# Kernel optimization log

Hardware: AMD Instinct MI355X
Metric: run time of the kernel (lower is better)

The kernel has to match this reference:

```python
import jax, jax.numpy as jnp
import numpy as np

B, N, D, H = 4, 1024, 768, 12
HD = D // H
HID = 4 * D
EPS = 1e-5


def setup_inputs():
    key = jax.random.key(0)
    ks = iter(jax.random.split(key, 64))
    def rnd(*shape):
        return jax.random.normal(next(ks), shape, jnp.float32) * 0.02
    d = {
        "img_tok": jax.random.normal(next(ks), (B, N, D), jnp.float32),
        "evt_tok": jax.random.normal(next(ks), (B, N, D), jnp.float32),
    }
    for nm in ["ln_q1", "ln_kv1", "ln_q2", "ln_kv2", "ln_mi", "ln_me"]:
        d[nm + "_g"] = jnp.ones((D,), jnp.float32)
        d[nm + "_b"] = jnp.zeros((D,), jnp.float32)
    for p in ["si", "se"]:
        d[p + "_qkv_w"] = rnd(D, 3 * D)
        d[p + "_qkv_b"] = jnp.zeros((3 * D,), jnp.float32)
        d[p + "_proj_w"] = rnd(D, D)
        d[p + "_proj_b"] = jnp.zeros((D,), jnp.float32)
    for p in ["xei", "xie"]:
        for m in ["q", "k", "v", "p"]:
            d[p + "_" + m + "_w"] = rnd(D, D)
            d[p + "_" + m + "_b"] = jnp.zeros((D,), jnp.float32)
    for p in ["mi", "me"]:
        d[p + "_fc1_w"] = rnd(D, HID)
        d[p + "_fc1_b"] = jnp.zeros((HID,), jnp.float32)
        d[p + "_fc2_w"] = rnd(HID, D)
        d[p + "_fc2_b"] = jnp.zeros((D,), jnp.float32)
    return d


def _ln(x, g, b):
    m = jnp.mean(x, -1, keepdims=True)
    v = jnp.mean((x - m) ** 2, -1, keepdims=True)
    return (x - m) * jax.lax.rsqrt(v + EPS) * g + b


def _self_attn(x, qkv_w, qkv_b, p_w, p_b):
    qkv = (x @ qkv_w + qkv_b).reshape(B, N, 3, H, HD)
    q, k, v = qkv[:, :, 0], qkv[:, :, 1], qkv[:, :, 2]  # each (B,N,H,HD)
    s = jnp.einsum("bqhd,bkhd->bhqk", q, k) * (HD ** -0.5)
    a = jax.nn.softmax(s, -1)
    o = jnp.einsum("bhqk,bkhd->bqhd", a, v).reshape(B, N, D)
    return o @ p_w + p_b


def _cross_attn(qx, kvx, q_w, q_b, k_w, k_b, v_w, v_b, p_w, p_b):
    q = (qx @ q_w + q_b).reshape(B, N, H, HD)
    k = (kvx @ k_w + k_b).reshape(B, N, H, HD)
    v = (kvx @ v_w + v_b).reshape(B, N, H, HD)
    # invert_softmax=True: negate scores before softmax
    s = -(jnp.einsum("bqhd,bkhd->bhqk", q, k) * (HD ** -0.5))
    a = jax.nn.softmax(s, -1)
    o = jnp.einsum("bhqk,bkhd->bqhd", a, v).reshape(B, N, D)
    return o @ p_w + p_b


def _mlp(x, w1, b1, w2, b2):
    return jax.nn.gelu(x @ w1 + b1, approximate=False) @ w2 + b2


def _fwd(img_tok, evt_tok,
         ln_q1_g, ln_q1_b, ln_kv1_g, ln_kv1_b,
         si_qkv_w, si_qkv_b, si_proj_w, si_proj_b,
         se_qkv_w, se_qkv_b, se_proj_w, se_proj_b,
         ln_q2_g, ln_q2_b, ln_kv2_g, ln_kv2_b,
         xei_q_w, xei_q_b, xei_k_w, xei_k_b, xei_v_w, xei_v_b, xei_p_w, xei_p_b,
         xie_q_w, xie_q_b, xie_k_w, xie_k_b, xie_v_w, xie_v_b, xie_p_w, xie_p_b,
         ln_mi_g, ln_mi_b, mi_fc1_w, mi_fc1_b, mi_fc2_w, mi_fc2_b,
         ln_me_g, ln_me_b, me_fc1_w, me_fc1_b, me_fc2_w, me_fc2_b):
    img = img_tok + _self_attn(_ln(img_tok, ln_q1_g, ln_q1_b),
                               si_qkv_w, si_qkv_b, si_proj_w, si_proj_b)
    evt = evt_tok + _self_attn(_ln(evt_tok, ln_kv1_g, ln_kv1_b),
                               se_qkv_w, se_qkv_b, se_proj_w, se_proj_b)
    i1, e1 = img, evt
    # shared norm_q2 / norm_kv2 weights across both cross-attn directions
    img = i1 + _cross_attn(_ln(i1, ln_q2_g, ln_q2_b), _ln(e1, ln_kv2_g, ln_kv2_b),
                           xei_q_w, xei_q_b, xei_k_w, xei_k_b, xei_v_w, xei_v_b,
                           xei_p_w, xei_p_b)
    evt = e1 + _cross_attn(_ln(e1, ln_q2_g, ln_q2_b), _ln(i1, ln_kv2_g, ln_kv2_b),
                           xie_q_w, xie_q_b, xie_k_w, xie_k_b, xie_v_w, xie_v_b,
                           xie_p_w, xie_p_b)
    img = img + _mlp(_ln(img, ln_mi_g, ln_mi_b), mi_fc1_w, mi_fc1_b, mi_fc2_w, mi_fc2_b)
    evt = evt + _mlp(_ln(evt, ln_me_g, ln_me_b), me_fc1_w, me_fc1_b, me_fc2_w, me_fc2_b)
    return img, evt


def reference(img_tok, evt_tok,
              ln_q1_g, ln_q1_b, ln_kv1_g, ln_kv1_b,
              si_qkv_w, si_qkv_b, si_proj_w, si_proj_b,
              se_qkv_w, se_qkv_b, se_proj_w, se_proj_b,
              ln_q2_g, ln_q2_b, ln_kv2_g, ln_kv2_b,
              xei_q_w, xei_q_b, xei_k_w, xei_k_b, xei_v_w, xei_v_b, xei_p_w, xei_p_b,
              xie_q_w, xie_q_b, xie_k_w, xie_k_b, xie_v_w, xie_v_b, xie_p_w, xie_p_b,
              ln_mi_g, ln_mi_b, mi_fc1_w, mi_fc1_b, mi_fc2_w, mi_fc2_b,
              ln_me_g, ln_me_b, me_fc1_w, me_fc1_b, me_fc2_w, me_fc2_b):
    return _fwd(img_tok, evt_tok,
                ln_q1_g, ln_q1_b, ln_kv1_g, ln_kv1_b,
                si_qkv_w, si_qkv_b, si_proj_w, si_proj_b,
                se_qkv_w, se_qkv_b, se_proj_w, se_proj_b,
                ln_q2_g, ln_q2_b, ln_kv2_g, ln_kv2_b,
                xei_q_w, xei_q_b, xei_k_w, xei_k_b, xei_v_w, xei_v_b, xei_p_w, xei_p_b,
                xie_q_w, xie_q_b, xie_k_w, xie_k_b, xie_v_w, xie_v_b, xie_p_w, xie_p_b,
                ln_mi_g, ln_mi_b, mi_fc1_w, mi_fc1_b, mi_fc2_w, mi_fc2_b,
                ln_me_g, ln_me_b, me_fc1_w, me_fc1_b, me_fc2_w, me_fc2_b)
```

## Files before the change

kernel.cpp:

```cpp
#include <hip/hip_runtime.h>

constexpr int cB  = 4;
constexpr int cN  = 1024;
constexpr int cD  = 768;
constexpr int cH  = 12;
constexpr int cHD = 64;
constexpr int cHID = 3072;
constexpr int cBN = cB * cN;

typedef __attribute__((ext_vector_type(8))) short bf16x8;
typedef __attribute__((ext_vector_type(4))) float f32x4;

static __device__ __forceinline__ unsigned short f2bf(float f) {
    union { float f; unsigned int u; } v; v.f = f;
    unsigned int u = v.u;
    return (unsigned short)((u + 0x7FFFu + ((u >> 16) & 1u)) >> 16);
}

static __device__ __forceinline__ float gelu_as(float v) {
    float w  = v * 0.70710678118f;
    float aw = fabsf(w);
    float t  = __builtin_amdgcn_rcpf(fmaf(aw, 0.3275911f, 1.0f));
    float p  = t * fmaf(t, fmaf(t, fmaf(t, fmaf(t, 1.061405429f, -1.453152027f),
                                        1.421413741f), -0.284496736f), 0.254829592f);
    float e  = __builtin_amdgcn_exp2f(w * w * -1.44269504f);
    float ea = fmaf(-p, e, 1.0f);
    float er = __builtin_copysignf(ea, w);
    return 0.5f * v * (1.0f + er);
}

static __device__ __forceinline__ void gl_lds16(const void* g, void* l) {
    __builtin_amdgcn_global_load_lds(
        (const __attribute__((address_space(1))) unsigned int*)g,
        (__attribute__((address_space(3))) unsigned int*)l, 16, 0, 0);
}

struct WcTab {
    const float* src[16];
    unsigned long long dstoff[16];
    int K[16];
    int N[16];
    int start[17];
};

__global__ __launch_bounds__(256)
void wconv_all(WcTab tab, unsigned short* __restrict__ WoBase) {
    int b = blockIdx.x;
    int i = 0;
    while (i < 15 && b >= tab.start[i + 1]) i++;
    const float* __restrict__ W = tab.src[i];
    unsigned short* __restrict__ Wo = WoBase + tab.dstoff[i];
    int K = tab.K[i], N = tab.N[i];
    int tb = b - tab.start[i];
    int Kt = K >> 6;
    int k0 = (tb % Kt) * 64, n0 = (tb / Kt) * 64;

    __shared__ float Ls[64][68];
    int t = threadIdx.x;
    int lr = t >> 4, lc = (t & 15) * 4;
    #pragma unroll
    for (int q = 0; q < 4; q++) {
        float4 v = *(const float4*)&W[(size_t)(k0 + lr + q * 16) * N + n0 + lc];
        Ls[lr + q * 16][lc + 0] = v.x;  Ls[lr + q * 16][lc + 1] = v.y;
        Ls[lr + q * 16][lc + 2] = v.z;  Ls[lr + q * 16][lc + 3] = v.w;
    }
    __syncthreads();
    int mt = t >> 3;
    int nb = mt & 3, kb = mt >> 2;
    int sub = t & 7;
    int K8 = K >> 3;
    size_t chunk = ((size_t)(n0 / 16 + nb) * K8 + (size_t)(k0 / 8 + kb)) * 128;
    unsigned short buf[16];
    #pragma unroll
    for (int rr = 0; rr < 2; rr++) {
        int n_r = sub * 2 + rr;
        #pragma unroll
        for (int kk = 0; kk < 8; kk++)
            buf[rr * 8 + kk] = f2bf(Ls[kb * 8 + kk][nb * 16 + n_r]);
    }
    uint4 w0, w1;
    w0.x = buf[0] | ((unsigned)buf[1] << 16);   w0.y = buf[2] | ((unsigned)buf[3] << 16);
    w0.z = buf[4] | ((unsigned)buf[5] << 16);   w0.w = buf[6] | ((unsigned)buf[7] << 16);
    w1.x = buf[8] | ((unsigned)buf[9] << 16);   w1.y = buf[10] | ((unsigned)buf[11] << 16);
    w1.z = buf[12] | ((unsigned)buf[13] << 16); w1.w = buf[14] | ((unsigned)buf[15] << 16);
    *(uint4*)&Wo[chunk + sub * 16]     = w0;
    *(uint4*)&Wo[chunk + sub * 16 + 8] = w1;
}

static __device__ __forceinline__ void ln_body(const float* __restrict__ x,
                                               const float* __restrict__ g,
                                               const float* __restrict__ b,
                                               unsigned short* __restrict__ y,
                                               int R) {
    __shared__ float psum[16][17], psq[16][17];
    __shared__ float mean_s[16], rstd_s[16];
    int t = threadIdx.x;
    int r = t >> 4, c16 = t & 15;
    const float* xr = x + ((size_t)R * 16 + r) * cD;
    float s = 0.f, sq = 0.f;
    #pragma unroll
    for (int i = 0; i < 12; i++) {
        float4 v = *(const float4*)&xr[c16 * 4 + i * 64];
        s  += v.x + v.y + v.z + v.w;
        sq += v.x * v.x + v.y * v.y + v.z * v.z + v.w * v.w;
    }
    psum[r][c16] = s; psq[r][c16] = sq;
    __syncthreads();
    if (t < 16) {
        float ss = 0.f, qq = 0.f;
        #pragma unroll
        for (int i = 0; i < 16; i++) { ss += psum[t][i]; qq += psq[t][i]; }
        float m = ss / (float)cD;
        mean_s[t] = m;
        rstd_s[t] = rsqrtf(qq / (float)cD - m * m + 1e-5f);
    }
    __syncthreads();
    int r2 = t & 15, cslot = t >> 4;
    const float* xr2 = x + ((size_t)R * 16 + r2) * cD;
    float m = mean_s[r2], rs = rstd_s[r2];
    for (int c = cslot; c < 96; c += 16) {
        float4 a0 = *(const float4*)&xr2[c * 8];
        float4 a1 = *(const float4*)&xr2[c * 8 + 4];
        float4 g0 = *(const float4*)&g[c * 8];
        float4 g1 = *(const float4*)&g[c * 8 + 4];
        float4 b0 = *(const float4*)&b[c * 8];
        float4 b1 = *(const float4*)&b[c * 8 + 4];
        unsigned short o[8];
        o[0] = f2bf((a0.x - m) * rs * g0.x + b0.x);
        o[1] = f2bf((a0.y - m) * rs * g0.y + b0.y);
        o[2] = f2bf((a0.z - m) * rs * g0.z + b0.z);
        o[3] = f2bf((a0.w - m) * rs * g0.w + b0.w);
        o[4] = f2bf((a1.x - m) * rs * g1.x + b1.x);
        o[5] = f2bf((a1.y - m) * rs * g1.y + b1.y);
        o[6] = f2bf((a1.z - m) * rs * g1.z + b1.z);
        o[7] = f2bf((a1.w - m) * rs * g1.w + b1.w);
        uint4 w;
        w.x = o[0] | ((unsigned)o[1] << 16); w.y = o[2] | ((unsigned)o[3] << 16);
        w.z = o[4] | ((unsigned)o[5] << 16); w.w = o[6] | ((unsigned)o[7] << 16);
        *(uint4*)&y[((size_t)R * 96 + c) * 128 + r2 * 8] = w;
    }
}

struct LnTab {
    const float* x[4];
    const float* g[4];
    const float* b[4];
    unsigned short* y[4];
};

__global__ __launch_bounds__(256)
void ln4_kernel(LnTab T) {
    int s = blockIdx.x >> 8;
    ln_body(T.x[s], T.g[s], T.b[s], T.y[s], blockIdx.x & 255);
}

struct GPair {
    const unsigned short* A0;  const unsigned short* A1;
    const unsigned short* B0;  const unsigned short* B1;
    const float* bias0;        const float* bias1;
    const float* biasB0;       const float* biasB1;
    const float* res0;         const float* res1;
    void* C0;                  void* C1;
    unsigned short* V0;        unsigned short* V1;
};

template<int NBUF, int KS>
__global__ __launch_bounds__(256, 4)
void mfma_gemm(GPair P, int K, int N, int ostride, int vsplit, int mode) {
    constexpr int KC   = KS / 8;
    constexpr int ASL  = 128 * KS / 8;
    constexpr int BSL  = 64 * KS / 8;
    constexpr int LPA  = ASL / 256;
    constexpr int LPB  = BSL / 256;
    constexpr int AH   = NBUF - 1;
    constexpr int NSUB = KS / 32;
    __shared__ bf16x8 aT[NBUF][ASL];
    __shared__ bf16x8 bT[NBUF][BSL];

    int z = blockIdx.z;
    const unsigned short* A   = z ? P.A1 : P.A0;
    const unsigned short* Bw  = z ? P.B1 : P.B0;
    const float* bias  = z ? P.bias1  : P.bias0;
    const float* biasB = z ? P.biasB1 : P.biasB0;
    const float* res   = z ? P.res1   : P.res0;
    void* Cout         = z ? P.C1     : P.C0;
    unsigned short* VtOut = z ? P.V1  : P.V0;

    int t = threadIdx.x;
    int w = t >> 6, l = t & 63;
    int la = l & 15, lb = l >> 4;
    int m0 = blockIdx.x * 128, n0 = blockIdx.y * 64;
    int K8 = K >> 3;

    f32x4 acc[2][4];
    #pragma unroll
    for (int i = 0; i < 2; i++)
        #pragma unroll
        for (int j = 0; j < 4; j++) acc[i][j] = (f32x4){0.f, 0.f, 0.f, 0.f};

    const unsigned short* pA[LPA];
    #pragma unroll
    for (int q = 0; q < LPA; q++) {
        int slot = w * (LPA * 64) + q * 64 + l;
        int ci = slot >> 4, sub = slot & 15;
        int mi = ci / KC, kb = ci % KC;
        pA[q] = A + (((size_t)((m0 >> 4) + mi)) * K8 + kb) * 128 + sub * 8;
    }
    const unsigned short* pB[LPB];
    #pragma unroll
    for (int q = 0; q < LPB; q++) {
        int slot = w * (LPB * 64) + q * 64 + l;
        int ci = slot >> 4, sub = slot & 15;
        int nj = ci / KC, kb = ci % KC;
        pB[q] = Bw + (((size_t)((n0 >> 4) + nj)) * K8 + kb) * 128 + sub * 8;
    }

    auto stage = [&](int buf, int step) {
        size_t off = (size_t)step * (KS * 16);
        #pragma unroll
        for (int q = 0; q < LPA; q++)
            gl_lds16(pA[q] + off, &aT[buf][w * (LPA * 64) + q * 64]);
        #pragma unroll
        for (int q = 0; q < LPB; q++)
            gl_lds16(pB[q] + off, &bT[buf][w * (LPB * 64) + q * 64]);
    };

    int nsteps = K / KS;
    #pragma unroll
    for (int p = 0; p < AH; p++) stage(p, p);
    for (int s = 0; s < nsteps; s++) {
        int cb = s % NBUF;
        int rem = nsteps - 1 - s;
        if (s + AH < nsteps) {
            stage((s + AH) % NBUF, s + AH);
            asm volatile("s_waitcnt vmcnt(6)" ::: "memory");
        } else if (rem == 2) {
            asm volatile("s_waitcnt vmcnt(6)" ::: "memory");
        } else if (rem == 1) {
            asm volatile("s_waitcnt vmcnt(3)" ::: "memory");
        } else {
            asm volatile("s_waitcnt vmcnt(0)" ::: "memory");
        }
        __builtin_amdgcn_s_barrier();

        #pragma unroll
        for (int kk = 0; kk < NSUB; kk++) {
            bf16x8 av[2], bv[4];
            #pragma unroll
            for (int i = 0; i < 2; i++)
                av[i] = aT[cb][((2 * w + i) * KC + kk * 4 + lb) * 16 + la];
            #pragma unroll
            for (int j = 0; j < 4; j++)
                bv[j] = bT[cb][(j * KC + kk * 4 + lb) * 16 + la];
            #pragma unroll
            for (int i = 0; i < 2; i++)
                #pragma unroll
                for (int j = 0; j < 4; j++)
                    acc[i][j] = __builtin_amdgcn_mfma_f32_16x16x32_bf16(av[i], bv[j], acc[i][j], 0, 0, 0);
        }

        asm volatile("s_waitcnt lgkmcnt(0)" ::: "memory");
        __builtin_amdgcn_s_barrier();
    }

    int col = l & 15;
    int rb = (l >> 4) * 4;
    int mw = m0 + w * 32;
    if (mode == 2) {
        float* out = (float*)Cout;
        #pragma unroll
        for (int j = 0; j < 4; j++) {
            int n = n0 + j * 16 + col;
            float bj = bias[n];
            #pragma unroll
            for (int i = 0; i < 2; i++)
                #pragma unroll
                for (int r = 0; r < 4; r++) {
                    int mm = mw + i * 16 + rb + r;
                    out[(size_t)mm * ostride + n] = acc[i][j][r] + bj + res[(size_t)mm * ostride + n];
                }
        }
    } else if (mode == 1) {
        unsigned short* out = (unsigned short*)Cout;
        int N8 = N >> 3;
        #pragma unroll
        for (int j = 0; j < 4; j++) {
            int n = n0 + j * 16 + col;
            float bj = bias[n];
            #pragma unroll
            for (int i = 0; i < 2; i++)
                #pragma unroll
                for (int r = 0; r < 4; r++) {
                    int mm = mw + i * 16 + rb + r;
                    float v = gelu_as(acc[i][j][r] + bj);
                    size_t ad = ((size_t)(mm >> 4) * N8 + (n >> 3)) * 128 + (mm & 15) * 8 + (n & 7);
                    out[ad] = f2bf(v);
                }
        }
    } else {
        bool toVt = (mode == 3) && (n0 >= vsplit);
        if (!toVt) {
            unsigned short* out = (unsigned short*)Cout;
            #pragma unroll
            for (int j = 0; j < 4; j++) {
                int n = n0 + j * 16 + col;
                float bj = bias[n];
                #pragma unroll
                for (int i = 0; i < 2; i++)
                    #pragma unroll
                    for (int r = 0; r < 4; r++) {
                        int mm = mw + i * 16 + rb + r;
                        out[(size_t)mm * ostride + n] = f2bf(acc[i][j][r] + bj);
                    }
            }
        } else {
            #pragma unroll
            for (int j = 0; j < 4; j++) {
                int n = n0 + j * 16 + col;
                int vc = n - vsplit;
                float bj = biasB[vc];
                int ph = vc >> 6, d = vc & 63;
                #pragma unroll
                for (int i = 0; i < 2; i++) {
                    int mm = mw + i * 16 + rb;
                    int bbv = mm >> 10, tok = mm & 1023;
                    unsigned short q0 = f2bf(acc[i][j][0] + bj);
                    unsigned short q1 = f2bf(acc[i][j][1] + bj);
                    unsigned short q2 = f2bf(acc[i][j][2] + bj);
                    unsigned short q3 = f2bf(acc[i][j][3] + bj);
                    uint2 pk;
                    pk.x = q0 | ((unsigned)q1 << 16);
                    pk.y = q2 | ((unsigned)q3 << 16);
                    size_t ad = ((size_t)(bbv * 12 + ph) * 64 + d) * 1024 + tok;
                    *(uint2*)&VtOut[ad] = pk;
                }
            }
        }
    }
}

__global__ __launch_bounds__(256, 2)
void fattn_kernel(const unsigned short* __restrict__ Q0,
                  const unsigned short* __restrict__ Q1,
                  const unsigned short* __restrict__ Kq0,
                  const unsigned short* __restrict__ Kq1,
                  const unsigned short* __restrict__ Vt0,
                  const unsigned short* __restrict__ Vt1,
                  unsigned short* __restrict__ Oo0,
                  unsigned short* __restrict__ Oo1,
                  int qk_stride, float scale) {
    __shared__ unsigned short Kls[2][4096];
    __shared__ unsigned short Vls[2][4096];
    __shared__ unsigned short Ps[4][16][72];

    int z = blockIdx.z;
    const unsigned short* Qp = z ? Q1 : Q0;
    const unsigned short* Kp = z ? Kq1 : Kq0;
    const unsigned short* Vt = z ? Vt1 : Vt0;
    unsigned short* O        = z ? Oo1 : Oo0;

    int t = threadIdx.x;
    int w = t >> 6, l = t & 63;
    int la = l & 15, lb = l >> 4;
    int swz = la & 7;
    int blk = blockIdx.x;
    int qt0 = (blk & 15) * 64 + w * 16;
    int bh = blk >> 4;
    int h = bh % cH, bb = bh / cH;

    const unsigned short* Qb = Qp + (size_t)(bb * cN) * qk_stride + h * cHD;
    const unsigned short* Kb = Kp + (size_t)(bb * cN) * qk_stride + h * cHD;
    const unsigned short* Vb = Vt + (size_t)(bb * cH + h) * (64 * 1024);

    bf16x8 av[2];
    #pragma unroll
    for (int s = 0; s < 2; s++)
        av[s] = *(const bf16x8*)(Qb + (size_t)(qt0 + la) * qk_stride + 32 * s + 8 * lb);

    int ch0 = w * 128 + l;
    int ch1 = ch0 + 64;
    int r0 = ch0 >> 3, c0 = (ch0 & 7) ^ (r0 & 7);
    int r1 = ch1 >> 3, c1 = (ch1 & 7) ^ (r1 & 7);
    const unsigned short* K0 = Kb + (size_t)r0 * qk_stride + c0 * 8;
    const unsigned short* K1 = Kb + (size_t)r1 * qk_stride + c1 * 8;
    const unsigned short* V0 = Vb + (size_t)r0 * 1024 + c0 * 8;
    const unsigned short* V1 = Vb + (size_t)r1 * 1024 + c1 * 8;
    int dst0 = w * 1024;
    int dst1 = dst0 + 512;

    auto stage = [&](int buf, int kt0) {
        gl_lds16(K0 + (size_t)kt0 * qk_stride, &Kls[buf][dst0]);
        gl_lds16(K1 + (size_t)kt0 * qk_stride, &Kls[buf][dst1]);
        gl_lds16(V0 + kt0, &Vls[buf][dst0]);
        gl_lds16(V1 + kt0, &Vls[buf][dst1]);
    };

    const float sc2 = scale * 1.44269504f;
    bf16x8 ones;
    #pragma unroll
    for (int e = 0; e < 8; e++) ones[e] = (short)0x3F80;

    float m2[4];
    f32x4 acc_o[4], acc_l;
    #pragma unroll
    for (int r = 0; r < 4; r++) m2[r] = -1e30f;
    acc_l = (f32x4){0.f, 0.f, 0.f, 0.f};
    #pragma unroll
    for (int nt = 0; nt < 4; nt++) acc_o[nt] = (f32x4){0.f, 0.f, 0.f, 0.f};

    stage(0, 0);
    for (int it = 0; it < 16; it++) {
        int cb = it & 1;
        if (it < 15) {
            stage(cb ^ 1, (it + 1) << 6);
            asm volatile("s_waitcnt vmcnt(4)" ::: "memory");
        } else {
            asm volatile("s_waitcnt vmcnt(0)" ::: "memory");
        }
        __builtin_amdgcn_s_barrier();
        asm volatile("" ::: "memory");

        bf16x8 kf[4][2];
        #pragma unroll
        for (int j = 0; j < 4; j++)
            #pragma unroll
            for (int s = 0; s < 2; s++)
                kf[j][s] = *(const bf16x8*)&Kls[cb][(16 * j + la) * 64 + (((4 * s + lb) ^ swz) << 3)];

        f32x4 sj[4];
        #pragma unroll
        for (int j = 0; j < 4; j++) sj[j] = (f32x4){0.f, 0.f, 0.f, 0.f};
        #pragma unroll
        for (int j = 0; j < 4; j++)
            #pragma unroll
            for (int s = 0; s < 2; s++)
                sj[j] = __builtin_amdgcn_mfma_f32_16x16x32_bf16(av[s], kf[j][s], sj[j], 0, 0, 0);

        float x2[4][4];
        #pragma unroll
        for (int j = 0; j < 4; j++)
            #pragma unroll
            for (int r = 0; r < 4; r++) x2[j][r] = sj[j][r] * sc2;

        float p[4][4];
        #pragma unroll
        for (int j = 0; j < 4; j++)
            #pragma unroll
            for (int r = 0; r < 4; r++)
                p[j][r] = __builtin_amdgcn_exp2f(x2[j][r] - m2[r]);

        float mt2[4];
        #pragma unroll
        for (int r = 0; r < 4; r++)
            mt2[r] = fmaxf(fmaxf(x2[0][r], x2[1][r]), fmaxf(x2[2][r], x2[3][r]));
        #pragma unroll
        for (int off = 1; off <= 8; off <<= 1)
            #pragma unroll
            for (int r = 0; r < 4; r++)
                mt2[r] = fmaxf(mt2[r], __shfl_xor(mt2[r], off, 64));

        int ok = (mt2[0] <= m2[0] + 11.f) && (mt2[1] <= m2[1] + 11.f) &&
                 (mt2[2] <= m2[2] + 11.f) && (mt2[3] <= m2[3] + 11.f);
        if (!__all(ok)) {
            #pragma unroll
            for (int r = 0; r < 4; r++) {
                float mn = fmaxf(m2[r], mt2[r]);
                float al = __builtin_amdgcn_exp2f(m2[r] - mn);
                acc_l[r] *= al;
                #pragma unroll
                for (int nt = 0; nt < 4; nt++) acc_o[nt][r] *= al;
                m2[r] = mn;
            }
            #pragma unroll
            for (int j = 0; j < 4; j++)
                #pragma unroll
                for (int r = 0; r < 4; r++)
                    p[j][r] = __builtin_amdgcn_exp2f(x2[j][r] - m2[r]);
        }

        #pragma unroll
        for (int j = 0; j < 4; j++)
            #pragma unroll
            for (int rp = 0; rp < 2; rp++) {
                unsigned u;
                asm("v_cvt_pk_bf16_f32 %0, %1, %2"
                    : "=v"(u) : "v"(p[j][2 * rp]), "v"(p[j][2 * rp + 1]));
                Ps[w][lb * 4 + 2 * rp][16 * j + la]     = (unsigned short)u;
                Ps[w][lb * 4 + 2 * rp + 1][16 * j + la] = (unsigned short)(u >> 16);
            }
        asm volatile("s_waitcnt lgkmcnt(0)" ::: "memory");
        bf16x8 pf[2];
        #pragma unroll
        for (int s = 0; s < 2; s++)
            pf[s] = *(const bf16x8*)&Ps[w][la][32 * s + 8 * lb];

        bf16x8 vf[4][2];
        #pragma unroll
        for (int nt = 0; nt < 4; nt++)
            #pragma unroll
            for (int s = 0; s < 2; s++)
                vf[nt][s] = *(const bf16x8*)&Vls[cb][(16 * nt + la) * 64 + (((4 * s + lb) ^ swz) << 3)];
        #pragma unroll
        for (int nt = 0; nt < 4; nt++)
            #pragma unroll
            for (int s = 0; s < 2; s++)
                acc_o[nt] = __builtin_amdgcn_mfma_f32_16x16x32_bf16(pf[s], vf[nt][s], acc_o[nt], 0, 0, 0);
        #pragma unroll
        for (int s = 0; s < 2; s++)
            acc_l = __builtin_amdgcn_mfma_f32_16x16x32_bf16(pf[s], ones, acc_l, 0, 0, 0);

        asm volatile("s_waitcnt lgkmcnt(0)" ::: "memory");
        __builtin_amdgcn_s_barrier();
    }

    float inv[4];
    #pragma unroll
    for (int r = 0; r < 4; r++) inv[r] = 1.0f / acc_l[r];
    size_t mhi = ((size_t)bb * cN + qt0) >> 4;
    #pragma unroll
    for (int nt = 0; nt < 4; nt++) {
        int k = h * cHD + 16 * nt + la;
        size_t base = (mhi * 96 + (k >> 3)) * 128 + (k & 7);
        #pragma unroll
        for (int r = 0; r < 4; r++) {
            unsigned short val = f2bf(acc_o[nt][r] * inv[r]);
            O[base + (lb * 4 + r) * 8] = val;
        }
    }
}

extern "C" void kernel_launch(void* const* d_in, const int* in_sizes, int n_in,
                              void* d_out, int out_size, void* d_ws, size_t ws_size,
                              hipStream_t stream) {
    const float* img_tok  = (const float*)d_in[0];
    const float* evt_tok  = (const float*)d_in[1];
    const float* ln_q1_g  = (const float*)d_in[2];
    const float* ln_q1_b  = (const float*)d_in[3];
    const float* ln_kv1_g = (const float*)d_in[4];
    const float* ln_kv1_b = (const float*)d_in[5];
    const float* ln_q2_g  = (const float*)d_in[6];
    const float* ln_q2_b  = (const float*)d_in[7];
    const float* ln_kv2_g = (const float*)d_in[8];
    const float* ln_kv2_b = (const float*)d_in[9];
    const float* ln_mi_g  = (const float*)d_in[10];
    const float* ln_mi_b  = (const float*)d_in[11];
    const float* ln_me_g  = (const float*)d_in[12];
    const float* ln_me_b  = (const float*)d_in[13];
    const float* si_qkv_w  = (const float*)d_in[14];
    const float* si_qkv_b  = (const float*)d_in[15];
    const float* si_proj_w = (const float*)d_in[16];
    const float* si_proj_b = (const float*)d_in[17];
    const float* se_qkv_w  = (const float*)d_in[18];
    const float* se_qkv_b  = (const float*)d_in[19];
    const float* se_proj_w = (const float*)d_in[20];
    const float* se_proj_b = (const float*)d_in[21];
    const float* xei_q_w = (const float*)d_in[22];
    const float* xei_q_b = (const float*)d_in[23];
    const float* xei_k_w = (const float*)d_in[24];
    const float* xei_k_b = (const float*)d_in[25];
    const float* xei_v_w = (const float*)d_in[26];
    const float* xei_v_b = (const float*)d_in[27];
    const float* xei_p_w = (const float*)d_in[28];
    const float* xei_p_b = (const float*)d_in[29];
    const float* xie_q_w = (const float*)d_in[30];
    const float* xie_q_b = (const float*)d_in[31];
    const float* xie_k_w = (const float*)d_in[32];
    const float* xie_k_b = (const float*)d_in[33];
    const float* xie_v_w = (const float*)d_in[34];
    const float* xie_v_b = (const float*)d_in[35];
    const float* xie_p_w = (const float*)d_in[36];
    const float* xie_p_b = (const float*)d_in[37];
    const float* mi_fc1_w = (const float*)d_in[38];
    const float* mi_fc1_b = (const float*)d_in[39];
    const float* mi_fc2_w = (const float*)d_in[40];
    const float* mi_fc2_b = (const float*)d_in[41];
    const float* me_fc1_w = (const float*)d_in[42];
    const float* me_fc1_b = (const float*)d_in[43];
    const float* me_fc2_w = (const float*)d_in[44];
    const float* me_fc2_b = (const float*)d_in[45];

    const size_t U = (size_t)cBN * cD;
    unsigned short* wsb = (unsigned short*)d_ws;
    unsigned short* Wz  = wsb;
    unsigned short* LNo = wsb + 18874368;
    unsigned short* AO  = LNo + U;
    unsigned short* T1  = AO + U;
    unsigned short* Vt  = T1 + 3 * U;
    unsigned short* T1b  = Vt + U;
    unsigned short* Vtb  = T1b + 3 * U;
    unsigned short* Hidb = Vtb + U;
    float* out_img = (float*)d_out;
    float* out_evt = out_img + U;

    const bool big = ws_size >= (size_t)(18874368 + 14 * U) * 2;

    const size_t O_SI_QKV = 0,        O_SE_QKV = 1769472;
    const size_t O_SI_P   = 3538944,  O_SE_P   = 4128768;
    const size_t O_XEI_Q  = 4718592,  O_XEI_KV = 5308416, O_XEI_P = 6488064;
    const size_t O_XIE_Q  = 7077888,  O_XIE_KV = 7667712, O_XIE_P = 8847360;
    const size_t O_MI_F1  = 9437184,  O_MI_F2  = 11796480;
    const size_t O_ME_F1  = 14155776, O_ME_F2  = 16515072;

    {
        WcTab tab;
        const float* srcs[16] = { si_qkv_w, se_qkv_w, si_proj_w, se_proj_w,
                                  xei_q_w, xei_k_w, xei_v_w, xei_p_w,
                                  xie_q_w, xie_k_w, xie_v_w, xie_p_w,
                                  mi_fc1_w, mi_fc2_w, me_fc1_w, me_fc2_w };
        const size_t offs[16] = { O_SI_QKV, O_SE_QKV, O_SI_P, O_SE_P,
                                  O_XEI_Q, O_XEI_KV, O_XEI_KV + 589824, O_XEI_P,
                                  O_XIE_Q, O_XIE_KV, O_XIE_KV + 589824, O_XIE_P,
                                  O_MI_F1, O_MI_F2, O_ME_F1, O_ME_F2 };
        const int Ks[16] = { 768, 768, 768, 768, 768, 768, 768, 768,
                             768, 768, 768, 768, 768, 3072, 768, 3072 };
        const int Ns[16] = { 2304, 2304, 768, 768, 768, 768, 768, 768,
                             768, 768, 768, 768, 3072, 768, 3072, 768 };
        int acc = 0;
        for (int i = 0; i < 16; i++) {
            tab.src[i] = srcs[i];
            tab.dstoff[i] = offs[i];
            tab.K[i] = Ks[i];
            tab.N[i] = Ns[i];
            tab.start[i] = acc;
            acc += (Ks[i] / 64) * (Ns[i] / 64);
        }
        tab.start[16] = acc;
        hipLaunchKernelGGL(wconv_all, dim3(acc), dim3(256), 0, stream, tab, Wz);
    }

    const float SC = 0.125f;

    auto lnN = [&](int nsets, const float* x0, const float* g0, const float* b0, unsigned short* y0,
                   const float* x1, const float* g1, const float* b1, unsigned short* y1,
                   const float* x2, const float* g2, const float* b2, unsigned short* y2,
                   const float* x3, const float* g3, const float* b3, unsigned short* y3) {
        LnTab T = {{x0, x1, x2, x3}, {g0, g1, g2, g3}, {b0, b1, b2, b3}, {y0, y1, y2, y3}};
        hipLaunchKernelGGL(ln4_kernel, dim3(nsets * 256), dim3(256), 0, stream, T);
    };
    auto gemm2 = [&](dim3 grid, GPair P, int K_, int N_, int ostride_, int vsplit_, int mode_) {
        int blocks = grid.x * grid.y * grid.z;
        if (blocks <= 768)
            hipLaunchKernelGGL((mfma_gemm<2, 64>), grid, dim3(256), 0, stream, P, K_, N_, ostride_, vsplit_, mode_);
        else
            hipLaunchKernelGGL((mfma_gemm<3, 32>), grid, dim3(256), 0, stream, P, K_, N_, ostride_, vsplit_, mode_);
    };
    auto attn2 = [&](int nz, const unsigned short* q0, const unsigned short* k0, const unsigned short* v0, unsigned short* o0,
                     const unsigned short* q1, const unsigned short* k1, const unsigned short* v1, unsigned short* o1,
                     float sc) {
        hipLaunchKernelGGL(fattn_kernel, dim3(cB * cH * 16, 1, nz), dim3(256), 0, stream,
                           q0, q1, k0, k1, v0, v1, o0, o1, 2304, sc);
    };

    if (big) {
        lnN(2, img_tok, ln_q1_g, ln_q1_b, LNo,  evt_tok, ln_kv1_g, ln_kv1_b, AO,
               img_tok, ln_q1_g, ln_q1_b, LNo,  img_tok, ln_q1_g, ln_q1_b, LNo);
        gemm2(dim3(32, 36, 2),
              {LNo, AO, Wz + O_SI_QKV, Wz + O_SE_QKV, si_qkv_b, se_qkv_b,
               si_qkv_b + 1536, se_qkv_b + 1536, nullptr, nullptr, T1, T1b, Vt, Vtb},
              768, 2304, 2304, 1536, 3);
        attn2(2, T1, T1 + 768, Vt, LNo,  T1b, T1b + 768, Vtb, AO, SC);
        gemm2(dim3(32, 12, 2),
              {LNo, AO, Wz + O_SI_P, Wz + O_SE_P, si_proj_b, se_proj_b,
               nullptr, nullptr, img_tok, evt_tok, out_img, out_evt, nullptr, nullptr},
              768, 768, 768, 0, 2);
        lnN(4, out_img, ln_q2_g, ln_q2_b, LNo,   out_evt, ln_kv2_g, ln_kv2_b, AO,
               out_img, ln_kv2_g, ln_kv2_b, Hidb, out_evt, ln_q2_g, ln_q2_b, Hidb + U);
        gemm2(dim3(32, 12, 2),
              {LNo, Hidb + U, Wz + O_XEI_Q, Wz + O_XIE_Q, xei_q_b, xie_q_b,
               nullptr, nullptr, nullptr, nullptr, T1, T1b, nullptr, nullptr},
              768, 768, 2304, 1 << 30, 0);
        gemm2(dim3(32, 24, 2),
              {AO, Hidb, Wz + O_XEI_KV, Wz + O_XIE_KV, xei_k_b, xie_k_b,
               xei_v_b, xie_v_b, nullptr, nullptr, T1 + 768, T1b + 768, Vt, Vtb},
              768, 1536, 2304, 768, 3);
        attn2(2, T1, T1 + 768, Vt, LNo,  T1b, T1b + 768, Vtb, AO, -SC);
        gemm2(dim3(32, 12, 2),
              {LNo, AO, Wz + O_XEI_P, Wz + O_XIE_P, xei_p_b, xie_p_b,
               nullptr, nullptr, out_img, out_evt, out_img, out_evt, nullptr, nullptr},
              768, 768, 768, 0, 2);
        lnN(2, out_img, ln_mi_g, ln_mi_b, LNo,  out_evt, ln_me_g, ln_me_b, AO,
               out_img, ln_mi_g, ln_mi_b, LNo,  out_img, ln_mi_g, ln_mi_b, LNo);
        gemm2(dim3(32, 48, 2),
              {LNo, AO, Wz + O_MI_F1, Wz + O_ME_F1, mi_fc1_b, me_fc1_b,
               nullptr, nullptr, nullptr, nullptr, T1, Hidb, nullptr, nullptr},
              768, 3072, 3072, 0, 1);
        gemm2(dim3(32, 12, 2),
              {T1, Hidb, Wz + O_MI_F2, Wz + O_ME_F2, mi_fc2_b, me_fc2_b,
               nullptr, nullptr, out_img, out_evt, out_img, out_evt, nullptr, nullptr},
              3072, 768, 768, 0, 2);
    } else {
        unsigned short* Hid = AO;
        auto ln1 = [&](const float* x_, const float* g_, const float* b_, unsigned short* y_) {
            lnN(1, x_, g_, b_, y_, x_, g_, b_, y_, x_, g_, b_, y_, x_, g_, b_, y_);
        };
        auto gemm1 = [&](const unsigned short* A_, size_t woff, const float* b_, const float* bB_,
                         const float* r_, void* C_, unsigned short* V_, int K_, int N_,
                         int ostride_, int vsplit_, int mode_) {
            gemm2(dim3(cBN / 128, N_ / 64, 1),
                  {A_, A_, Wz + woff, Wz + woff, b_, b_, bB_, bB_, r_, r_, C_, C_, V_, V_},
                  K_, N_, ostride_, vsplit_, mode_);
        };
        auto attn1 = [&](const unsigned short* q_, const unsigned short* k_,
                         unsigned short* o_, float sc_) {
            attn2(1, q_, k_, Vt, o_, q_, k_, Vt, o_, sc_);
        };

        ln1(img_tok, ln_q1_g, ln_q1_b, LNo);
        gemm1(LNo, O_SI_QKV, si_qkv_b, si_qkv_b + 1536, nullptr, T1, Vt, 768, 2304, 2304, 1536, 3);
        attn1(T1, T1 + 768, AO, SC);
        gemm1(AO, O_SI_P, si_proj_b, nullptr, img_tok, out_img, Vt, 768, 768, 768, 0, 2);

        ln1(evt_tok, ln_kv1_g, ln_kv1_b, LNo);
        gemm1(LNo, O_SE_QKV, se_qkv_b, se_qkv_b + 1536, nullptr, T1, Vt, 768, 2304, 2304, 1536, 3);
        attn1(T1, T1 + 768, AO, SC);
        gemm1(AO, O_SE_P, se_proj_b, nullptr, evt_tok, out_evt, Vt, 768, 768, 768, 0, 2);

        ln1(out_img, ln_q2_g, ln_q2_b, LNo);
        gemm1(LNo, O_XEI_Q, xei_q_b, nullptr, nullptr, T1, Vt, 768, 768, 2304, 1 << 30, 0);
        ln1(out_evt, ln_kv2_g, ln_kv2_b, LNo);
        gemm1(LNo, O_XEI_KV, xei_k_b, xei_v_b, nullptr, T1 + 768, Vt, 768, 1536, 2304, 768, 3);
        attn1(T1, T1 + 768, AO, -SC);

        ln1(out_img, ln_kv2_g, ln_kv2_b, LNo);
        gemm1(LNo, O_XIE_KV, xie_k_b, xie_v_b, nullptr, T1 + 768, Vt, 768, 1536, 2304, 768, 3);
        ln1(out_evt, ln_q2_g, ln_q2_b, LNo);
        gemm1(LNo, O_XIE_Q, xie_q_b, nullptr, nullptr, T1, Vt, 768, 768, 2304, 1 << 30, 0);

        gemm1(AO, O_XEI_P, xei_p_b, nullptr, out_img, out_img, Vt, 768, 768, 768, 0, 2);
        attn1(T1, T1 + 768, AO, -SC);
        gemm1(AO, O_XIE_P, xie_p_b, nullptr, out_evt, out_evt, Vt, 768, 768, 768, 0, 2);

        lnN(2, out_img, ln_mi_g, ln_mi_b, LNo,  out_evt, ln_me_g, ln_me_b, Vt,
               out_img, ln_mi_g, ln_mi_b, LNo,  out_img, ln_mi_g, ln_mi_b, LNo);
        gemm1(LNo, O_MI_F1, mi_fc1_b, nullptr, nullptr, Hid, Vt, 768, 3072, 3072, 0, 1);
        gemm1(Hid, O_MI_F2, mi_fc2_b, nullptr, out_img, out_img, Vt, 3072, 768, 768, 0, 2);
        gemm1(Vt,  O_ME_F1, me_fc1_b, nullptr, nullptr, Hid, Vt, 768, 3072, 3072, 0, 1);
        gemm1(Hid, O_ME_F2, me_fc2_b, nullptr, out_evt, out_evt, Vt, 3072, 768, 768, 0, 2);
    }
}
```

Before: 655.5 us.

## Process two 16-row query tiles per wave in flash attention

Each wave now handles 32 query rows as two 16-row sub-tiles, so a block covers 128 queries and the grid is halved. The K and V fragments loaded from LDS, along with the staged global loads, are reused across both sub-tiles, which cuts LDS reads and global K/V traffic per query. The cost is higher register pressure from the doubled accumulators and score arrays, which may limit occupancy under launch_bounds(256,2). It also leaves fewer blocks to fill the GPU.

```diff
diff --git a/kernel.cpp b/kernel.cpp
--- a/kernel.cpp
+++ b/kernel.cpp
@@ -351,7 +351,7 @@
                   int qk_stride, float scale) {
     __shared__ unsigned short Kls[2][4096];
     __shared__ unsigned short Vls[2][4096];
-    __shared__ unsigned short Ps[4][16][72];
+    __shared__ unsigned short Ps[4][32][72];
 
     int z = blockIdx.z;
     const unsigned short* Qp = z ? Q1 : Q0;
@@ -364,18 +364,20 @@
     int la = l & 15, lb = l >> 4;
     int swz = la & 7;
     int blk = blockIdx.x;
-    int qt0 = (blk & 15) * 64 + w * 16;
-    int bh = blk >> 4;
+    int qt0 = (blk & 7) * 128 + w * 32;
+    int bh = blk >> 3;
     int h = bh % cH, bb = bh / cH;
 
     const unsigned short* Qb = Qp + (size_t)(bb * cN) * qk_stride + h * cHD;
     const unsigned short* Kb = Kp + (size_t)(bb * cN) * qk_stride + h * cHD;
     const unsigned short* Vb = Vt + (size_t)(bb * cH + h) * (64 * 1024);
 
-    bf16x8 av[2];
-    #pragma unroll
-    for (int s = 0; s < 2; s++)
-        av[s] = *(const bf16x8*)(Qb + (size_t)(qt0 + la) * qk_stride + 32 * s + 8 * lb);
+    bf16x8 av[2][2];
+    #pragma unroll
+    for (int u = 0; u < 2; u++)
+        #pragma unroll
+        for (int s = 0; s < 2; s++)
+            av[u][s] = *(const bf16x8*)(Qb + (size_t)(qt0 + u * 16 + la) * qk_stride + 32 * s + 8 * lb);
 
     int ch0 = w * 128 + l;
     int ch1 = ch0 + 64;
@@ -400,13 +402,16 @@
     #pragma unroll
     for (int e = 0; e < 8; e++) ones[e] = (short)0x3F80;
 
-    float m2[4];
-    f32x4 acc_o[4], acc_l;
-    #pragma unroll
-    for (int r = 0; r < 4; r++) m2[r] = -1e30f;
-    acc_l = (f32x4){0.f, 0.f, 0.f, 0.f};
-    #pragma unroll
-    for (int nt = 0; nt < 4; nt++) acc_o[nt] = (f32x4){0.f, 0.f, 0.f, 0.f};
+    float m2[2][4];
+    f32x4 acc_o[2][4], acc_l[2];
+    #pragma unroll
+    for (int u = 0; u < 2; u++) {
+        #pragma unroll
+        for (int r = 0; r < 4; r++) m2[u][r] = -1e30f;
+        acc_l[u] = (f32x4){0.f, 0.f, 0.f, 0.f};
+        #pragma unroll
+        for (int nt = 0; nt < 4; nt++) acc_o[u][nt] = (f32x4){0.f, 0.f, 0.f, 0.f};
+    }
 
     stage(0, 0);
     for (int it = 0; it < 16; it++) {
@@ -427,72 +432,81 @@
             for (int s = 0; s < 2; s++)
                 kf[j][s] = *(const bf16x8*)&Kls[cb][(16 * j + la) * 64 + (((4 * s + lb) ^ swz) << 3)];
 
-        f32x4 sj[4];
-        #pragma unroll
-        for (int j = 0; j < 4; j++) sj[j] = (f32x4){0.f, 0.f, 0.f, 0.f};
+        f32x4 sj[2][4];
+        #pragma unroll
+        for (int u = 0; u < 2; u++)
+            #pragma unroll
+            for (int j = 0; j < 4; j++) sj[u][j] = (f32x4){0.f, 0.f, 0.f, 0.f};
         #pragma unroll
         for (int j = 0; j < 4; j++)
             #pragma unroll
             for (int s = 0; s < 2; s++)
-                sj[j] = __builtin_amdgcn_mfma_f32_16x16x32_bf16(av[s], kf[j][s], sj[j], 0, 0, 0);
-
-        float x2[4][4];
-        #pragma unroll
-        for (int j = 0; j < 4; j++)
-            #pragma unroll
-            for (int r = 0; r < 4; r++) x2[j][r] = sj[j][r] * sc2;
-
-        float p[4][4];
-        #pragma unroll
-        for (int j = 0; j < 4; j++)
+                #pragma unroll
+                for (int u = 0; u < 2; u++)
+                    sj[u][j] = __builtin_amdgcn_mfma_f32_16x16x32_bf16(av[u][s], kf[j][s], sj[u][j], 0, 0, 0);
+
+        #pragma unroll
+        for (int u = 0; u < 2; u++) {
+            float x2[4][4];
+            #pragma unroll
+            for (int j = 0; j < 4; j++)
+                #pragma unroll
+                for (int r = 0; r < 4; r++) x2[j][r] = sj[u][j][r] * sc2;
+
+            float p[4][4];
+            #pragma unroll
+            for (int j = 0; j < 4; j++)
+                #pragma unroll
+                for (int r = 0; r < 4; r++)
+                    p[j][r] = __builtin_amdgcn_exp2f(x2[j][r] - m2[u][r]);
+
+            float mt2[4];
             #pragma unroll
             for (int r = 0; r < 4; r++)
-                p[j][r] = __builtin_amdgcn_exp2f(x2[j][r] - m2[r]);
-
-        float mt2[4];
-        #pragma unroll
-        for (int r = 0; r < 4; r++)
-            mt2[r] = fmaxf(fmaxf(x2[0][r], x2[1][r]), fmaxf(x2[2][r], x2[3][r]));
-        #pragma unroll
-        for (int off = 1; off <= 8; off <<= 1)
-            #pragma unroll
-            for (int r = 0; r < 4; r++)
-                mt2[r] = fmaxf(mt2[r], __shfl_xor(mt2[r], off, 64));
-
-        int ok = (mt2[0] <= m2[0] + 11.f) && (mt2[1] <= m2[1] + 11.f) &&
-                 (mt2[2] <= m2[2] + 11.f) && (mt2[3] <= m2[3] + 11.f);
-        if (!__all(ok)) {
-            #pragma unroll
-            for (int r = 0; r < 4; r++) {
-                float mn = fmaxf(m2[r], mt2[r]);
-                float al = __builtin_amdgcn_exp2f(m2[r] - mn);
-                acc_l[r] *= al;
-                #pragma unroll
-                for (int nt = 0; nt < 4; nt++) acc_o[nt][r] *= al;
-                m2[r] = mn;
+                mt2[r] = fmaxf(fmaxf(x2[0][r], x2[1][r]), fmaxf(x2[2][r], x2[3][r]));
+            #pragma unroll
+            for (int off = 1; off <= 8; off <<= 1)
+                #pragma unroll
+                for (int r = 0; r < 4; r++)
+                    mt2[r] = fmaxf(mt2[r], __shfl_xor(mt2[r], off, 64));
+
+            int ok = (mt2[0] <= m2[u][0] + 11.f) && (mt2[1] <= m2[u][1] + 11.f) &&
+                     (mt2[2] <= m2[u][2] + 11.f) && (mt2[3] <= m2[u][3] + 11.f);
+            if (!__all(ok)) {
+                #pragma unroll
+                for (int r = 0; r < 4; r++) {
+                    float mn = fmaxf(m2[u][r], mt2[r]);
+                    float al = __builtin_amdgcn_exp2f(m2[u][r] - mn);
+                    acc_l[u][r] *= al;
+                    #pragma unroll
+                    for (int nt = 0; nt < 4; nt++) acc_o[u][nt][r] *= al;
+                    m2[u][r] = mn;
+                }
+                #pragma unroll
+                for (int j = 0; j < 4; j++)
+                    #pragma unroll
+                    for (int r = 0; r < 4; r++)
+                        p[j][r] = __builtin_amdgcn_exp2f(x2[j][r] - m2[u][r]);
             }
+
             #pragma unroll
             for (int j = 0; j < 4; j++)
                 #pragma unroll
-                for (int r = 0; r < 4; r++)
-                    p[j][r] = __builtin_amdgcn_exp2f(x2[j][r] - m2[r]);
-        }
-
-        #pragma unroll
-        for (int j = 0; j < 4; j++)
-            #pragma unroll
-            for (int rp = 0; rp < 2; rp++) {
-                unsigned u;
-                asm("v_cvt_pk_bf16_f32 %0, %1, %2"
-                    : "=v"(u) : "v"(p[j][2 * rp]), "v"(p[j][2 * rp + 1]));
-                Ps[w][lb * 4 + 2 * rp][16 * j + la]     = (unsigned short)u;
-                Ps[w][lb * 4 + 2 * rp + 1][16 * j + la] = (unsigned short)(u >> 16);
-            }
+                for (int rp = 0; rp < 2; rp++) {
+                    unsigned uw;
+                    asm("v_cvt_pk_bf16_f32 %0, %1, %2"
+                        : "=v"(uw) : "v"(p[j][2 * rp]), "v"(p[j][2 * rp + 1]));
+                    Ps[w][u * 16 + lb * 4 + 2 * rp][16 * j + la]     = (unsigned short)uw;
+                    Ps[w][u * 16 + lb * 4 + 2 * rp + 1][16 * j + la] = (unsigned short)(uw >> 16);
+                }
+        }
         asm volatile("s_waitcnt lgkmcnt(0)" ::: "memory");
-        bf16x8 pf[2];
-        #pragma unroll
-        for (int s = 0; s < 2; s++)
-            pf[s] = *(const bf16x8*)&Ps[w][la][32 * s + 8 * lb];
+        bf16x8 pf[2][2];
+        #pragma unroll
+        for (int u = 0; u < 2; u++)
+            #pragma unroll
+            for (int s = 0; s < 2; s++)
+                pf[u][s] = *(const bf16x8*)&Ps[w][u * 16 + la][32 * s + 8 * lb];
 
         bf16x8 vf[4][2];
         #pragma unroll
@@ -504,27 +518,34 @@
         for (int nt = 0; nt < 4; nt++)
             #pragma unroll
             for (int s = 0; s < 2; s++)
-                acc_o[nt] = __builtin_amdgcn_mfma_f32_16x16x32_bf16(pf[s], vf[nt][s], acc_o[nt], 0, 0, 0);
+                #pragma unroll
+                for (int u = 0; u < 2; u++)
+                    acc_o[u][nt] = __builtin_amdgcn_mfma_f32_16x16x32_bf16(pf[u][s], vf[nt][s], acc_o[u][nt], 0, 0, 0);
         #pragma unroll
         for (int s = 0; s < 2; s++)
-            acc_l = __builtin_amdgcn_mfma_f32_16x16x32_bf16(pf[s], ones, acc_l, 0, 0, 0);
+            #pragma unroll
+            for (int u = 0; u < 2; u++)
+                acc_l[u] = __builtin_amdgcn_mfma_f32_16x16x32_bf16(pf[u][s], ones, acc_l[u], 0, 0, 0);
 
         asm volatile("s_waitcnt lgkmcnt(0)" ::: "memory");
         __builtin_amdgcn_s_barrier();
     }
 
-    float inv[4];
-    #pragma unroll
-    for (int r = 0; r < 4; r++) inv[r] = 1.0f / acc_l[r];
-    size_t mhi = ((size_t)bb * cN + qt0) >> 4;
-    #pragma unroll
-    for (int nt = 0; nt < 4; nt++) {
-        int k = h * cHD + 16 * nt + la;
-        size_t base = (mhi * 96 + (k >> 3)) * 128 + (k & 7);
-        #pragma unroll
-        for (int r = 0; r < 4; r++) {
-            unsigned short val = f2bf(acc_o[nt][r] * inv[r]);
-            O[base + (lb * 4 + r) * 8] = val;
+    #pragma unroll
+    for (int u = 0; u < 2; u++) {
+        float inv[4];
+        #pragma unroll
+        for (int r = 0; r < 4; r++) inv[r] = 1.0f / acc_l[u][r];
+        size_t mhi = ((size_t)bb * cN + qt0 + u * 16) >> 4;
+        #pragma unroll
+        for (int nt = 0; nt < 4; nt++) {
+            int k = h * cHD + 16 * nt + la;
+            size_t base = (mhi * 96 + (k >> 3)) * 128 + (k & 7);
+            #pragma unroll
+            for (int r = 0; r < 4; r++) {
+                unsigned short val = f2bf(acc_o[u][nt][r] * inv[r]);
+                O[base + (lb * 4 + r) * 8] = val;
+            }
         }
     }
 }
@@ -647,7 +668,7 @@
     auto attn2 = [&](int nz, const unsigned short* q0, const unsigned short* k0, const unsigned short* v0, unsigned short* o0,
                      const unsigned short* q1, const unsigned short* k1, const unsigned short* v1, unsigned short* o1,
                      float sc) {
-        hipLaunchKernelGGL(fattn_kernel, dim3(cB * cH * 16, 1, nz), dim3(256), 0, stream,
+        hipLaunchKernelGGL(fattn_kernel, dim3(cB * cH * 8, 1, nz), dim3(256), 0, stream,
                            q0, q1, k0, k1, v0, v1, o0, o1, 2304, sc);
     };
 
```

Result: faster. 625.5 us (-4.6%).
